# Kernel optimization log

Hardware: AMD Instinct MI355X
Metric: run time of the kernel (lower is better)

## Reference

```python
import jax, jax.numpy as jnp
import numpy as np

VOCAB, EMB, HID, OUT = 32000, 512, 1024, 1
B, S = 128, 512


def setup_inputs() -> dict:
    key = jax.random.key(0)
    ks = jax.random.split(key, 8)
    x = jax.random.randint(ks[0], (B, S), 0, VOCAB, dtype=jnp.int64 if jax.config.jax_enable_x64 else jnp.int32)
    emb = jax.random.normal(ks[1], (VOCAB, EMB), dtype=jnp.float32)
    # torch Linear stores weight as [out, in], y = x @ W.T + b
    W_w = jax.random.normal(ks[2], (HID, EMB), dtype=jnp.float32) * (1.0 / np.sqrt(EMB))
    W_b = jax.random.normal(ks[3], (HID,), dtype=jnp.float32) * 0.01
    U_w = jax.random.normal(ks[4], (HID, HID), dtype=jnp.float32) * (1.0 / np.sqrt(HID))
    U_b = jax.random.normal(ks[5], (HID,), dtype=jnp.float32) * 0.01
    V_w = jax.random.normal(ks[6], (OUT, HID), dtype=jnp.float32) * (1.0 / np.sqrt(HID))
    V_b = jax.random.normal(ks[7], (OUT,), dtype=jnp.float32) * 0.01
    return {"x": x, "emb": emb, "W_w": W_w, "W_b": W_b, "U_w": U_w, "U_b": U_b, "V_w": V_w, "V_b": V_b}


def reference(x, emb, W_w, W_b, U_w, U_b, V_w, V_b):
    xe = emb[x]  # [B, S, E] embedding lookup
    # Precompute input projection for all timesteps (same math as per-step W(x_t))
    pre = jnp.einsum('bse,he->bsh', xe, W_w) + W_b  # [B, S, H]

    def step(h, p_t):
        # h_t = tanh(W x_t + b_W + U h_{t-1} + b_U)
        h_new = jnp.tanh(p_t + h @ U_w.T + U_b)
        return h_new, None

    h0 = jnp.zeros((x.shape[0], U_w.shape[0]), dtype=pre.dtype)
    hT, _ = jax.lax.scan(step, h0, jnp.swapaxes(pre, 0, 1))  # scan over seq
    logits = hT @ V_w.T + V_b  # [B, OUT]
    return jax.nn.sigmoid(logits)
```

## Files before the change

### kernel.cpp

```cpp
#include <hip/hip_runtime.h>
#include <hip/hip_bf16.h>

typedef short short8 __attribute__((ext_vector_type(8)));
typedef float f32x4 __attribute__((ext_vector_type(4)));

#define OFF_U   0x0UL
#define OFF_W   0x200000UL
#define OFF_PRE 0x300000UL
#define OFF_H0  0x8300000UL
#define OFF_H1  0x8340000UL
#define OFF_CNT 0x8380000UL

static __device__ __forceinline__ unsigned short f2bf(float f) {
  return __builtin_bit_cast(unsigned short, __float2bfloat16(f));
}
static __device__ __forceinline__ float bf2f(unsigned short u) {
  unsigned int v = (unsigned int)u << 16;
  return __builtin_bit_cast(float, v);
}
static __device__ __forceinline__ unsigned int pack2(float a, float b) {
  return (unsigned int)f2bf(a) | ((unsigned int)f2bf(b) << 16);
}
static __device__ __forceinline__ float fast_tanh(float x) {
  float xc = fminf(fmaxf(x, -10.f), 10.f);
  float e2 = __expf(2.f * xc);
  return 1.f - 2.f * __builtin_amdgcn_rcpf(e2 + 1.f);
}

__global__ __launch_bounds__(256) void cvt_bf16(const float* __restrict__ in,
                                                unsigned short* __restrict__ out, int n4) {
  int idx = blockIdx.x * 256 + threadIdx.x;
  if (idx < n4) {
    float4 v = *(const float4*)&in[idx * 4];
    uint2 p; p.x = pack2(v.x, v.y); p.y = pack2(v.z, v.w);
    *(uint2*)&out[idx * 4] = p;
  }
}

__global__ __launch_bounds__(256) void pre_gemm(const int* __restrict__ x,
                                                const float* __restrict__ emb,
                                                const unsigned short* __restrict__ Wbf,
                                                unsigned short* __restrict__ pre) {
  const int t   = blockIdx.y;
  const int n0  = blockIdx.x * 128;
  const int tid = threadIdx.x;
  const int lane = tid & 63, w = tid >> 6;
  const int q = lane >> 4, l15 = lane & 15;

  __shared__ unsigned short Alds[128][72];
  __shared__ unsigned short Blds[128][72];
  __shared__ int tok[128];
  if (tid < 128) tok[tid] = x[tid * 512 + t];
  __syncthreads();

  f32x4 acc[4][4];
  #pragma unroll
  for (int a = 0; a < 4; ++a)
    #pragma unroll
    for (int b = 0; b < 4; ++b) acc[a][b] = {0.f, 0.f, 0.f, 0.f};

  const int wm = (w & 1) * 64, wn = (w >> 1) * 64;

  for (int k0 = 0; k0 < 512; k0 += 64) {
    #pragma unroll
    for (int it = 0; it < 8; ++it) {
      int idx = it * 256 + tid;
      int r = idx >> 4, c4 = (idx & 15) * 4;
      float4 v = *(const float4*)&emb[tok[r] * 512 + k0 + c4];
      uint2 p; p.x = pack2(v.x, v.y); p.y = pack2(v.z, v.w);
      *(uint2*)&Alds[r][c4] = p;
    }
    #pragma unroll
    for (int it = 0; it < 4; ++it) {
      int idx = it * 256 + tid;
      int r = idx >> 3, c8 = (idx & 7) * 8;
      *(int4*)&Blds[r][c8] = *(const int4*)&Wbf[(n0 + r) * 512 + k0 + c8];
    }
    __syncthreads();
    #pragma unroll
    for (int kt = 0; kt < 2; ++kt) {
      short8 af[4], bfr[4];
      #pragma unroll
      for (int mt = 0; mt < 4; ++mt) af[mt]  = *(const short8*)&Alds[wm + mt*16 + l15][kt*32 + q*8];
      #pragma unroll
      for (int nt = 0; nt < 4; ++nt) bfr[nt] = *(const short8*)&Blds[wn + nt*16 + l15][kt*32 + q*8];
      #pragma unroll
      for (int mt = 0; mt < 4; ++mt)
        #pragma unroll
        for (int nt = 0; nt < 4; ++nt)
          acc[mt][nt] = __builtin_amdgcn_mfma_f32_16x16x32_bf16(af[mt], bfr[nt], acc[mt][nt], 0, 0, 0);
    }
    __syncthreads();
  }
  #pragma unroll
  for (int mt = 0; mt < 4; ++mt) {
    int brow = wm + mt * 16 + q * 4;
    #pragma unroll
    for (int nt = 0; nt < 4; ++nt) {
      int i = n0 + wn + nt * 16 + l15;
      #pragma unroll
      for (int r = 0; r < 4; ++r)
        pre[(t * 128 + brow + r) * 1024 + i] = f2bf(acc[mt][nt][r]);
    }
  }
}

__global__ __launch_bounds__(512, 2) void recurrence(const unsigned short* __restrict__ Ubf,
                                                     const unsigned short* __restrict__ pre,
                                                     const float* __restrict__ Wb,
                                                     const float* __restrict__ Ub,
                                                     unsigned short* __restrict__ h0buf,
                                                     unsigned short* __restrict__ h1buf,
                                                     unsigned int* __restrict__ cnt) {
  const int c   = blockIdx.x & 7;
  const int s   = blockIdx.x >> 3;
  const int tid = threadIdx.x;
  const int lane = tid & 63, wv = tid >> 6;
  const int q = lane >> 4, l15 = lane & 15;
  const int ibase = s * 128 + wv * 16;
  const int bglob = c * 16;

  __shared__ unsigned short hlds[16][1032];

  {
    int r = tid >> 5;
    int kk = (tid & 31) * 4;
    *(uint2*)&hlds[r][s * 128 + kk] = make_uint2(0u, 0u);
  }

  short8 A[32];
  {
    const unsigned short* Up = Ubf + (ibase + l15) * 1024 + q * 8;
    #pragma unroll
    for (int kt = 0; kt < 32; ++kt) A[kt] = *(const short8*)(Up + kt * 32);
  }
  #pragma unroll
  for (int kt = 0; kt < 32; ++kt) asm volatile("" : "+v"(A[kt]));

  float4 bias;
  {
    int i0 = ibase + q * 4;
    float4 wb = *(const float4*)&Wb[i0];
    float4 ub = *(const float4*)&Ub[i0];
    bias = make_float4(wb.x + ub.x, wb.y + ub.y, wb.z + ub.z, wb.w + ub.w);
  }

  unsigned int* fbase = cnt + c * 32;
  const bool pact = (lane < 8) && (lane != s);
  const unsigned int* fpoll = fbase + (lane & 7);
  unsigned int* fmine = fbase + s;
  const int sb = tid >> 7;
  const int sk = (tid & 127) * 8;
  const bool notown = (sk >> 7) != s;
  const unsigned short* prebase = pre + (size_t)(bglob + l15) * 1024 + ibase + q * 4;

  __syncthreads();

  #pragma unroll 1
  for (int t = 0; t < 512; ++t) {
    uint2 pvr;
    {
      const unsigned short* pp = prebase + (size_t)t * 131072;
      asm volatile("global_load_dwordx2 %0, %1, off" : "=v"(pvr) : "v"(pp));
    }

    const unsigned short* hprev = (t & 1) ? h1buf : h0buf;
    unsigned short* hnew        = (t & 1) ? h0buf : h1buf;

    if (t > 0) {
      if (wv == 0) {
        const unsigned int tt = (unsigned int)t;
        unsigned int va, vb;
        asm volatile("global_load_dword %0, %1, off sc1" : "=v"(va) : "v"(fpoll));
        for (;;) {
          asm volatile("global_load_dword %0, %1, off sc1\n\ts_waitcnt vmcnt(1)"
                       : "=v"(vb) : "v"(fpoll));
          unsigned int x = pact ? va : tt;
          if (__ballot(x < tt) == 0) break;
          asm volatile("global_load_dword %0, %1, off sc1\n\ts_waitcnt vmcnt(1)"
                       : "=v"(va) : "v"(fpoll));
          x = pact ? vb : tt;
          if (__ballot(x < tt) == 0) break;
        }
        asm volatile("s_waitcnt vmcnt(0)");
      }
      __syncthreads();
    }

    {
      const unsigned short* hp = hprev + (size_t)(bglob + sb) * 1024 + sk;
      int4 r0, r1, r2, r3;
      if (notown) {
        asm volatile(
          "global_load_dwordx4 %0, %4, off sc1\n\t"
          "global_load_dwordx4 %1, %5, off sc1\n\t"
          "global_load_dwordx4 %2, %6, off sc1\n\t"
          "global_load_dwordx4 %3, %7, off sc1"
          : "=&v"(r0), "=&v"(r1), "=&v"(r2), "=&v"(r3)
          : "v"(hp), "v"(hp + 4 * 1024), "v"(hp + 8 * 1024), "v"(hp + 12 * 1024));
      }
      asm volatile("s_waitcnt vmcnt(0)");
      if (notown) {
        *(int4*)&hlds[sb][sk]      = r0;
        *(int4*)&hlds[sb + 4][sk]  = r1;
        *(int4*)&hlds[sb + 8][sk]  = r2;
        *(int4*)&hlds[sb + 12][sk] = r3;
      }
    }
    __syncthreads();

    f32x4 acc0 = {0.f, 0.f, 0.f, 0.f}, acc1 = {0.f, 0.f, 0.f, 0.f};
    #pragma unroll
    for (int kt = 0; kt < 32; kt += 2) {
      short8 b0 = *(const short8*)&hlds[l15][kt * 32 + q * 8];
      short8 b1 = *(const short8*)&hlds[l15][kt * 32 + 32 + q * 8];
      acc0 = __builtin_amdgcn_mfma_f32_16x16x32_bf16(A[kt],     b0, acc0, 0, 0, 0);
      acc1 = __builtin_amdgcn_mfma_f32_16x16x32_bf16(A[kt + 1], b1, acc1, 0, 0, 0);
    }
    __syncthreads();

    float p0 = bf2f((unsigned short)(pvr.x & 0xffff));
    float p1 = bf2f((unsigned short)(pvr.x >> 16));
    float p2 = bf2f((unsigned short)(pvr.y & 0xffff));
    float p3 = bf2f((unsigned short)(pvr.y >> 16));
    float x0 = acc0[0] + acc1[0] + p0 + bias.x;
    float x1 = acc0[1] + acc1[1] + p1 + bias.y;
    float x2 = acc0[2] + acc1[2] + p2 + bias.z;
    float x3 = acc0[3] + acc1[3] + p3 + bias.w;
    uint2 pk;
    pk.x = pack2(fast_tanh(x0), fast_tanh(x1));
    pk.y = pack2(fast_tanh(x2), fast_tanh(x3));

    {
      const int i0 = ibase + q * 4;
      *(uint2*)&hlds[l15][i0] = pk;
      unsigned short* dst = hnew + (size_t)(bglob + l15) * 1024 + i0;
      asm volatile("global_store_dwordx2 %0, %1, off sc1\n\ts_waitcnt vmcnt(0)"
                   : : "v"(dst), "v"(pk));
    }
    __syncthreads();
    if (tid == 0) {
      unsigned int tv = (unsigned int)(t + 1);
      asm volatile("global_store_dword %0, %1, off sc1" : : "v"(fmine), "v"(tv));
    }
  }
}

__global__ __launch_bounds__(64) void final_out(const unsigned short* __restrict__ hT,
                                                const float* __restrict__ Vw,
                                                const float* __restrict__ Vb,
                                                float* __restrict__ out) {
  int b = blockIdx.x, lane = threadIdx.x;
  float sum = 0.f;
  #pragma unroll
  for (int k = 0; k < 16; ++k) {
    int i = k * 64 + lane;
    sum += bf2f(hT[b * 1024 + i]) * Vw[i];
  }
  #pragma unroll
  for (int off = 32; off; off >>= 1) sum += __shfl_down(sum, off);
  if (lane == 0) out[b] = 1.f / (1.f + expf(-(sum + Vb[0])));
}

extern "C" void kernel_launch(void* const* d_in, const int* in_sizes, int n_in,
                              void* d_out, int out_size, void* d_ws, size_t ws_size,
                              hipStream_t stream) {
  const int*   x   = (const int*)d_in[0];
  const float* emb = (const float*)d_in[1];
  const float* W_w = (const float*)d_in[2];
  const float* W_b = (const float*)d_in[3];
  const float* U_w = (const float*)d_in[4];
  const float* U_b = (const float*)d_in[5];
  const float* V_w = (const float*)d_in[6];
  const float* V_b = (const float*)d_in[7];
  float* out = (float*)d_out;
  char*  ws  = (char*)d_ws;

  unsigned short* Ubf = (unsigned short*)(ws + OFF_U);
  unsigned short* Wbf = (unsigned short*)(ws + OFF_W);
  unsigned short* pre = (unsigned short*)(ws + OFF_PRE);
  unsigned short* h0  = (unsigned short*)(ws + OFF_H0);
  unsigned short* h1  = (unsigned short*)(ws + OFF_H1);
  unsigned int*   cnt = (unsigned int*)(ws + OFF_CNT);

  hipMemsetAsync(ws + OFF_H0, 0, (OFF_CNT - OFF_H0) + 0x1000, stream);

  cvt_bf16<<<1024, 256, 0, stream>>>(U_w, Ubf, 1024 * 1024 / 4);
  cvt_bf16<<<512, 256, 0, stream>>>(W_w, Wbf, 1024 * 512 / 4);

  pre_gemm<<<dim3(8, 512), 256, 0, stream>>>(x, emb, Wbf, pre);

  void* args[] = {&Ubf, &pre, &W_b, &U_b, &h0, &h1, &cnt};
  hipLaunchCooperativeKernel((void*)recurrence, dim3(64), dim3(512), args, 0, stream);

  final_out<<<128, 64, 0, stream>>>(h0, V_w, V_b, out);
}
```

Before: 1.709 ms.

## Replace flag-counter barrier with epoch bits embedded in a 4-deep h ring

Removes the per-step flag store and flag polling. Instead, a 4-buffer ring of hidden states is used, and each bf16 value carries an epoch marker: bit 14, the top exponent bit, which is always zero for tanh outputs, is XOR-toggled every 4 steps. Readers spin directly on the h data until every element shows the expected epoch. This cuts one global round trip, the store-completion wait and a block barrier from each timestep. In exchange it relies on tanh output never setting that bit and on the ring depth being enough to prevent overwrite races. It also adds redundant re-reads of the full h tile while spinning.

```diff
diff --git a/kernel.cpp b/kernel.cpp
--- a/kernel.cpp
+++ b/kernel.cpp
@@ -7,9 +7,7 @@
 #define OFF_U   0x0UL
 #define OFF_W   0x200000UL
 #define OFF_PRE 0x300000UL
-#define OFF_H0  0x8300000UL
-#define OFF_H1  0x8340000UL
-#define OFF_CNT 0x8380000UL
+#define OFF_H   0x8300000UL
 
 static __device__ __forceinline__ unsigned short f2bf(float f) {
   return __builtin_bit_cast(unsigned short, __float2bfloat16(f));
@@ -109,9 +107,7 @@
                                                      const unsigned short* __restrict__ pre,
                                                      const float* __restrict__ Wb,
                                                      const float* __restrict__ Ub,
-                                                     unsigned short* __restrict__ h0buf,
-                                                     unsigned short* __restrict__ h1buf,
-                                                     unsigned int* __restrict__ cnt) {
+                                                     unsigned short* __restrict__ hb) {
   const int c   = blockIdx.x & 7;
   const int s   = blockIdx.x >> 3;
   const int tid = threadIdx.x;
@@ -145,10 +141,6 @@
     bias = make_float4(wb.x + ub.x, wb.y + ub.y, wb.z + ub.z, wb.w + ub.w);
   }
 
-  unsigned int* fbase = cnt + c * 32;
-  const bool pact = (lane < 8) && (lane != s);
-  const unsigned int* fpoll = fbase + (lane & 7);
-  unsigned int* fmine = fbase + s;
   const int sb = tid >> 7;
   const int sk = (tid & 127) * 8;
   const bool notown = (sk >> 7) != s;
@@ -164,47 +156,41 @@
       asm volatile("global_load_dwordx2 %0, %1, off" : "=v"(pvr) : "v"(pp));
     }
 
-    const unsigned short* hprev = (t & 1) ? h1buf : h0buf;
-    unsigned short* hnew        = (t & 1) ? h0buf : h1buf;
-
-    if (t > 0) {
-      if (wv == 0) {
-        const unsigned int tt = (unsigned int)t;
-        unsigned int va, vb;
-        asm volatile("global_load_dword %0, %1, off sc1" : "=v"(va) : "v"(fpoll));
-        for (;;) {
-          asm volatile("global_load_dword %0, %1, off sc1\n\ts_waitcnt vmcnt(1)"
-                       : "=v"(vb) : "v"(fpoll));
-          unsigned int x = pact ? va : tt;
-          if (__ballot(x < tt) == 0) break;
-          asm volatile("global_load_dword %0, %1, off sc1\n\ts_waitcnt vmcnt(1)"
-                       : "=v"(va) : "v"(fpoll));
-          x = pact ? vb : tt;
-          if (__ballot(x < tt) == 0) break;
-        }
-        asm volatile("s_waitcnt vmcnt(0)");
-      }
-      __syncthreads();
-    }
+    const unsigned short* hprev = hb + (size_t)((t + 3) & 3) * 131072;
+    unsigned short*       hnew  = hb + (size_t)(t & 3) * 131072;
+    const unsigned int et = (t == 0) ? 0u
+                          : (((((t - 1) >> 2) & 1) ^ 1) ? 0x40004000u : 0u);
 
     {
       const unsigned short* hp = hprev + (size_t)(bglob + sb) * 1024 + sk;
-      int4 r0, r1, r2, r3;
+      int4 d0, d1, d2, d3;
       if (notown) {
-        asm volatile(
-          "global_load_dwordx4 %0, %4, off sc1\n\t"
-          "global_load_dwordx4 %1, %5, off sc1\n\t"
-          "global_load_dwordx4 %2, %6, off sc1\n\t"
-          "global_load_dwordx4 %3, %7, off sc1"
-          : "=&v"(r0), "=&v"(r1), "=&v"(r2), "=&v"(r3)
-          : "v"(hp), "v"(hp + 4 * 1024), "v"(hp + 8 * 1024), "v"(hp + 12 * 1024));
-      }
-      asm volatile("s_waitcnt vmcnt(0)");
-      if (notown) {
-        *(int4*)&hlds[sb][sk]      = r0;
-        *(int4*)&hlds[sb + 4][sk]  = r1;
-        *(int4*)&hlds[sb + 8][sk]  = r2;
-        *(int4*)&hlds[sb + 12][sk] = r3;
+        for (;;) {
+          int4 r0, r1, r2, r3;
+          asm volatile(
+            "global_load_dwordx4 %0, %4, off sc1\n\t"
+            "global_load_dwordx4 %1, %5, off sc1\n\t"
+            "global_load_dwordx4 %2, %6, off sc1\n\t"
+            "global_load_dwordx4 %3, %7, off sc1\n\t"
+            "s_waitcnt vmcnt(0)"
+            : "=&v"(r0), "=&v"(r1), "=&v"(r2), "=&v"(r3)
+            : "v"(hp), "v"(hp + 4 * 1024), "v"(hp + 8 * 1024), "v"(hp + 12 * 1024));
+          d0.x = r0.x ^ (int)et; d0.y = r0.y ^ (int)et; d0.z = r0.z ^ (int)et; d0.w = r0.w ^ (int)et;
+          d1.x = r1.x ^ (int)et; d1.y = r1.y ^ (int)et; d1.z = r1.z ^ (int)et; d1.w = r1.w ^ (int)et;
+          d2.x = r2.x ^ (int)et; d2.y = r2.y ^ (int)et; d2.z = r2.z ^ (int)et; d2.w = r2.w ^ (int)et;
+          d3.x = r3.x ^ (int)et; d3.y = r3.y ^ (int)et; d3.z = r3.z ^ (int)et; d3.w = r3.w ^ (int)et;
+          unsigned int bad = (unsigned int)(d0.x | d0.y | d0.z | d0.w |
+                                            d1.x | d1.y | d1.z | d1.w |
+                                            d2.x | d2.y | d2.z | d2.w |
+                                            d3.x | d3.y | d3.z | d3.w) & 0x40004000u;
+          if (bad == 0) break;
+        }
+        *(int4*)&hlds[sb][sk]      = d0;
+        *(int4*)&hlds[sb + 4][sk]  = d1;
+        *(int4*)&hlds[sb + 8][sk]  = d2;
+        *(int4*)&hlds[sb + 12][sk] = d3;
+      } else {
+        asm volatile("s_waitcnt vmcnt(0)");
       }
     }
     __syncthreads();
@@ -232,16 +218,13 @@
     pk.y = pack2(fast_tanh(x2), fast_tanh(x3));
 
     {
+      const unsigned int tm = ((((t >> 2) & 1) ^ 1) ? 0x40004000u : 0u);
       const int i0 = ibase + q * 4;
       *(uint2*)&hlds[l15][i0] = pk;
+      uint2 pkt; pkt.x = pk.x ^ tm; pkt.y = pk.y ^ tm;
       unsigned short* dst = hnew + (size_t)(bglob + l15) * 1024 + i0;
-      asm volatile("global_store_dwordx2 %0, %1, off sc1\n\ts_waitcnt vmcnt(0)"
-                   : : "v"(dst), "v"(pk));
-    }
-    __syncthreads();
-    if (tid == 0) {
-      unsigned int tv = (unsigned int)(t + 1);
-      asm volatile("global_store_dword %0, %1, off sc1" : : "v"(fmine), "v"(tv));
+      asm volatile("global_store_dwordx2 %0, %1, off sc1"
+                   : : "v"(dst), "v"(pkt));
     }
   }
 }
@@ -279,19 +262,17 @@
   unsigned short* Ubf = (unsigned short*)(ws + OFF_U);
   unsigned short* Wbf = (unsigned short*)(ws + OFF_W);
   unsigned short* pre = (unsigned short*)(ws + OFF_PRE);
-  unsigned short* h0  = (unsigned short*)(ws + OFF_H0);
-  unsigned short* h1  = (unsigned short*)(ws + OFF_H1);
-  unsigned int*   cnt = (unsigned int*)(ws + OFF_CNT);
-
-  hipMemsetAsync(ws + OFF_H0, 0, (OFF_CNT - OFF_H0) + 0x1000, stream);
+  unsigned short* hb  = (unsigned short*)(ws + OFF_H);
+
+  hipMemsetAsync(ws + OFF_H, 0, 0x100000, stream);
 
   cvt_bf16<<<1024, 256, 0, stream>>>(U_w, Ubf, 1024 * 1024 / 4);
   cvt_bf16<<<512, 256, 0, stream>>>(W_w, Wbf, 1024 * 512 / 4);
 
   pre_gemm<<<dim3(8, 512), 256, 0, stream>>>(x, emb, Wbf, pre);
 
-  void* args[] = {&Ubf, &pre, &W_b, &U_b, &h0, &h1, &cnt};
+  void* args[] = {&Ubf, &pre, &W_b, &U_b, &hb};
   hipLaunchCooperativeKernel((void*)recurrence, dim3(64), dim3(512), args, 0, stream);
 
-  final_out<<<128, 64, 0, stream>>>(h0, V_w, V_b, out);
-}
+  final_out<<<128, 64, 0, stream>>>(hb + 3 * 131072, V_w, V_b, out);
+}
```

New measurement: 2.445 ms. +43.0%, slower.

## Embed step-parity tags in hidden-state bf16 data to drop store-completion wait

Applied to the files above, without the earlier changes.

Each stored bf16 hidden value has its top exponent bit XOR-tagged with a parity that alternates every two steps. That bit is always zero for tanh outputs, so it is free to carry the tag. Readers re-poll their global loads of neighbouring hidden slices until every tag matches, then untag the values before writing them to LDS. This lets the writer drop the s_waitcnt after its global store before raising the per-block step flag, removing one global-store round trip from the serial per-step critical path. In exchange it adds XOR and check work, possible retry loads, and correctness now depends on the tag encoding and on memory visibility ordering.

```diff
diff --git a/kernel.cpp b/kernel.cpp
--- a/kernel.cpp
+++ b/kernel.cpp
@@ -166,6 +166,8 @@
 
     const unsigned short* hprev = (t & 1) ? h1buf : h0buf;
     unsigned short* hnew        = (t & 1) ? h0buf : h1buf;
+    const unsigned int et = (t == 0) ? 0u
+                          : (((((t - 1) >> 1) & 1) ^ 1) ? 0x40004000u : 0u);
 
     if (t > 0) {
       if (wv == 0) {
@@ -189,22 +191,34 @@
 
     {
       const unsigned short* hp = hprev + (size_t)(bglob + sb) * 1024 + sk;
-      int4 r0, r1, r2, r3;
+      int4 d0, d1, d2, d3;
       if (notown) {
-        asm volatile(
-          "global_load_dwordx4 %0, %4, off sc1\n\t"
-          "global_load_dwordx4 %1, %5, off sc1\n\t"
-          "global_load_dwordx4 %2, %6, off sc1\n\t"
-          "global_load_dwordx4 %3, %7, off sc1"
-          : "=&v"(r0), "=&v"(r1), "=&v"(r2), "=&v"(r3)
-          : "v"(hp), "v"(hp + 4 * 1024), "v"(hp + 8 * 1024), "v"(hp + 12 * 1024));
-      }
-      asm volatile("s_waitcnt vmcnt(0)");
-      if (notown) {
-        *(int4*)&hlds[sb][sk]      = r0;
-        *(int4*)&hlds[sb + 4][sk]  = r1;
-        *(int4*)&hlds[sb + 8][sk]  = r2;
-        *(int4*)&hlds[sb + 12][sk] = r3;
+        for (;;) {
+          int4 r0, r1, r2, r3;
+          asm volatile(
+            "global_load_dwordx4 %0, %4, off sc1\n\t"
+            "global_load_dwordx4 %1, %5, off sc1\n\t"
+            "global_load_dwordx4 %2, %6, off sc1\n\t"
+            "global_load_dwordx4 %3, %7, off sc1\n\t"
+            "s_waitcnt vmcnt(0)"
+            : "=&v"(r0), "=&v"(r1), "=&v"(r2), "=&v"(r3)
+            : "v"(hp), "v"(hp + 4 * 1024), "v"(hp + 8 * 1024), "v"(hp + 12 * 1024));
+          d0.x = r0.x ^ (int)et; d0.y = r0.y ^ (int)et; d0.z = r0.z ^ (int)et; d0.w = r0.w ^ (int)et;
+          d1.x = r1.x ^ (int)et; d1.y = r1.y ^ (int)et; d1.z = r1.z ^ (int)et; d1.w = r1.w ^ (int)et;
+          d2.x = r2.x ^ (int)et; d2.y = r2.y ^ (int)et; d2.z = r2.z ^ (int)et; d2.w = r2.w ^ (int)et;
+          d3.x = r3.x ^ (int)et; d3.y = r3.y ^ (int)et; d3.z = r3.z ^ (int)et; d3.w = r3.w ^ (int)et;
+          unsigned int bad = (unsigned int)(d0.x | d0.y | d0.z | d0.w |
+                                            d1.x | d1.y | d1.z | d1.w |
+                                            d2.x | d2.y | d2.z | d2.w |
+                                            d3.x | d3.y | d3.z | d3.w) & 0x40004000u;
+          if (bad == 0) break;
+        }
+        *(int4*)&hlds[sb][sk]      = d0;
+        *(int4*)&hlds[sb + 4][sk]  = d1;
+        *(int4*)&hlds[sb + 8][sk]  = d2;
+        *(int4*)&hlds[sb + 12][sk] = d3;
+      } else {
+        asm volatile("s_waitcnt vmcnt(0)");
       }
     }
     __syncthreads();
@@ -232,11 +246,13 @@
     pk.y = pack2(fast_tanh(x2), fast_tanh(x3));
 
     {
+      const unsigned int tm = (((t >> 1) & 1) ^ 1) ? 0x40004000u : 0u;
       const int i0 = ibase + q * 4;
       *(uint2*)&hlds[l15][i0] = pk;
+      uint2 pkt; pkt.x = pk.x ^ tm; pkt.y = pk.y ^ tm;
       unsigned short* dst = hnew + (size_t)(bglob + l15) * 1024 + i0;
-      asm volatile("global_store_dwordx2 %0, %1, off sc1\n\ts_waitcnt vmcnt(0)"
-                   : : "v"(dst), "v"(pk));
+      asm volatile("global_store_dwordx2 %0, %1, off sc1"
+                   : : "v"(dst), "v"(pkt));
     }
     __syncthreads();
     if (tid == 0) {
```

Measured after the change: 1.589 ms. 7.1% less time.
